# Kernel tuning notes

Measured on AMD Instinct MI355X. Metric: run time of the kernel, lower is better.

The kernel has to match this reference:

```python
import jax, jax.numpy as jnp
import numpy as np

B, CIN, COUT, H, W, K, PAD = 8, 64, 64, 128, 128, 3, 1
KK = K * K


def setup_inputs() -> dict:
    key = jax.random.key(0)
    k1, k2, k3, k4 = jax.random.split(key, 4)
    x = jax.random.normal(k1, (B, CIN, H, W), jnp.float32)
    # offset/mask conv: 3*K*K output channels (2*KK offsets + KK mask logits).
    # Original zero-inits these; we use small random weights so the irregular
    # gather path is actually exercised (zero offsets degenerate to plain conv).
    w_off = jax.random.normal(k2, (3 * KK, CIN, K, K), jnp.float32) * 0.01
    b_off = jax.random.normal(k3, (3 * KK,), jnp.float32) * 0.01
    w_dcn = jax.random.normal(k4, (COUT, CIN, K, K), jnp.float32) * (1.0 / np.sqrt(CIN * KK))
    return {"x": x, "w_off": w_off, "b_off": b_off, "w_dcn": w_dcn}


def _bilinear_gather(x, py, px):
    # x: [B,C,H,W]; py/px: [B,KK,H,W] float sample coordinates.
    # Zero padding: integer corners outside the image contribute 0 (torchvision semantics).
    Bn, C, Hn, Wn = x.shape
    y0 = jnp.floor(py).astype(jnp.int32)
    x0 = jnp.floor(px).astype(jnp.int32)
    y1, x1 = y0 + 1, x0 + 1
    wy1 = py - y0.astype(py.dtype)
    wy0 = 1.0 - wy1
    wx1 = px - x0.astype(px.dtype)
    wx0 = 1.0 - wx1
    xf = x.reshape(Bn, C, Hn * Wn)

    def g(iy, ix):
        valid = ((iy >= 0) & (iy < Hn) & (ix >= 0) & (ix < Wn)).astype(x.dtype)
        idx = (jnp.clip(iy, 0, Hn - 1) * Wn + jnp.clip(ix, 0, Wn - 1)).reshape(Bn, -1)
        v = jax.vmap(lambda xr, i: xr[:, i])(xf, idx).reshape(Bn, C, *iy.shape[1:])
        return v * valid[:, None]  # [B,C,KK,H,W]

    return ((wy0 * wx0)[:, None] * g(y0, x0) + (wy0 * wx1)[:, None] * g(y0, x1)
            + (wy1 * wx0)[:, None] * g(y1, x0) + (wy1 * wx1)[:, None] * g(y1, x1))


def reference(x, w_off, b_off, w_dcn):
    dn = ('NCHW', 'OIHW', 'NCHW')
    off = jax.lax.conv_general_dilated(x, w_off, (1, 1), [(PAD, PAD), (PAD, PAD)],
                                       dimension_numbers=dn) + b_off[None, :, None, None]
    o1, o2, m = off[:, :KK], off[:, KK:2 * KK], off[:, 2 * KK:]
    mask = jax.nn.sigmoid(m)                    # [B,KK,H,W]
    offset = jnp.concatenate([o1, o2], axis=1)  # [B,2KK,H,W], torch cat((o1,o2),dim=1)
    # torchvision interprets channel 2k as dy, 2k+1 as dx for kernel point k
    dy, dx = offset[:, 0::2], offset[:, 1::2]   # each [B,KK,H,W]
    ki = (jnp.arange(KK) // K - PAD).astype(x.dtype)
    kj = (jnp.arange(KK) % K - PAD).astype(x.dtype)
    py = jnp.arange(H, dtype=x.dtype)[None, None, :, None] + ki[None, :, None, None] + dy
    px = jnp.arange(W, dtype=x.dtype)[None, None, None, :] + kj[None, :, None, None] + dx
    val = _bilinear_gather(x, py, px) * mask[:, None]  # [B,C,KK,H,W]
    return jnp.einsum('bckhw,ock->bohw', val, w_dcn.reshape(COUT, CIN, KK))
```

## Files before the change

### kernel.cpp

```cpp
#include <hip/hip_runtime.h>

#define Bn 8
#define CINn 64
#define COUTn 64
#define Hn 128
#define Wn 128
#define KKn 9

typedef __attribute__((ext_vector_type(8))) short short8v;
typedef __attribute__((ext_vector_type(4))) float f32x4;

__device__ __forceinline__ unsigned short f2bf(float f) {
    unsigned u = __float_as_uint(f);
    unsigned r = (u + 0x7FFFu + ((u >> 16) & 1u)) >> 16;
    return (unsigned short)r;
}

__global__ void wdcn_prep(const float* __restrict__ w_dcn, unsigned short* __restrict__ w2) {
    int i = blockIdx.x * 256 + threadIdx.x;
    if (i >= COUTn * CINn * KKn) return;
    int c = i & 63;
    int o = (i >> 6) & 63;
    int k = i >> 12;
    w2[i] = f2bf(w_dcn[(o * CINn + c) * KKn + k]);
}

__global__ void woffprep(const float* __restrict__ w_off, unsigned short* __restrict__ wofft) {
    int i = blockIdx.x * 256 + threadIdx.x;
    if (i >= 9 * 32 * 64) return;
    int c   = i & 63;
    int ch  = (i >> 6) & 31;
    int tap = i >> 11;
    wofft[i] = (ch < 27) ? f2bf(w_off[(ch * 64 + c) * 9 + tap]) : (unsigned short)0;
}

__launch_bounds__(256)
__global__ void offconv_mfma(const float* __restrict__ x,
                             const unsigned short* __restrict__ wofft,
                             const float* __restrict__ b_off, float* __restrict__ off) {
    __shared__ alignas(16) unsigned short XT[2 * 130 * 64];

    int blk = blockIdx.x;
    blk = (blk & 7) * 64 + (blk >> 3);
    const int b  = blk >> 6, hp = blk & 63;
    const int r0 = hp * 2;
    const int t  = threadIdx.x;
    const int lane = t & 63, wv = t >> 6;
    const int r16 = lane & 15, sub = lane >> 4;
    const int sw = t & 127, chalf = t >> 7;

    f32x4 acc[2][4];
#pragma unroll
    for (int mt = 0; mt < 2; ++mt)
#pragma unroll
        for (int nt = 0; nt < 4; ++nt) acc[mt][nt] = (f32x4){0.f, 0.f, 0.f, 0.f};

    if (t < 128) {
        int rs = t >> 6, which = (t >> 5) & 1, cpair = t & 31;
        int wslot = which ? 129 : 0;
        int c0 = cpair * 2;
        *(unsigned*)&XT[((rs * 130 + wslot) << 6) + (((c0 >> 3) ^ (wslot & 7)) << 3) + (c0 & 7)] = 0;
    }

    const float* xbase = x + (((long)b * CINn) << 14);

    for (int di = 0; di < 3; ++di) {
        if (di) __syncthreads();
#pragma unroll
        for (int rs = 0; rs < 2; ++rs) {
            int y = r0 + rs + di - 1;
            bool inb = (y >= 0 && y < Hn);
            int yc = inb ? y : 0;
            const float* xr = xbase + (yc << 7) + sw;
            int wslot = sw + 1;
#pragma unroll 4
            for (int cp = 0; cp < 16; ++cp) {
                int c0 = (chalf * 16 + cp) * 2;
                unsigned v = 0;
                if (inb) {
                    float lo = xr[(long)c0 << 14];
                    float hi = xr[(long)(c0 + 1) << 14];
                    v = (unsigned)f2bf(lo) | ((unsigned)f2bf(hi) << 16);
                }
                *(unsigned*)&XT[((rs * 130 + wslot) << 6) + (((c0 >> 3) ^ (wslot & 7)) << 3) + (c0 & 7)] = v;
            }
        }
        __syncthreads();

#pragma unroll
        for (int dj = 0; dj < 3; ++dj) {
            int tap = di * 3 + dj;
#pragma unroll
            for (int kk = 0; kk < 2; ++kk) {
                short8v a0 = *(const short8v*)(wofft + ((tap * 32 +      r16) << 6) + ((kk * 4 + sub) << 3));
                short8v a1 = *(const short8v*)(wofft + ((tap * 32 + 16 + r16) << 6) + ((kk * 4 + sub) << 3));
                short8v bfr[4];
#pragma unroll
                for (int nt = 0; nt < 4; ++nt) {
                    int ntile = wv * 4 + nt;
                    int hsel = ntile >> 3, wbase = (ntile & 7) * 16;
                    int wslot = wbase + r16 + dj;
                    int cchunk = kk * 4 + sub;
                    bfr[nt] = *(const short8v*)&XT[((hsel * 130 + wslot) << 6) + ((cchunk ^ (wslot & 7)) << 3)];
                }
#pragma unroll
                for (int nt = 0; nt < 4; ++nt) {
                    acc[0][nt] = __builtin_amdgcn_mfma_f32_16x16x32_bf16(a0, bfr[nt], acc[0][nt], 0, 0, 0);
                    acc[1][nt] = __builtin_amdgcn_mfma_f32_16x16x32_bf16(a1, bfr[nt], acc[1][nt], 0, 0, 0);
                }
            }
        }
    }

#pragma unroll
    for (int mt = 0; mt < 2; ++mt)
#pragma unroll
        for (int nt = 0; nt < 4; ++nt) {
            int ntile = wv * 4 + nt;
            int hsel = ntile >> 3, w = (ntile & 7) * 16 + r16;
            int h = r0 + hsel;
#pragma unroll
            for (int r = 0; r < 4; ++r) {
                int ch = mt * 16 + sub * 4 + r;
                if (ch < 27)
                    off[(((long)(b * 27 + ch)) << 14) + (h << 7) + w] = acc[mt][nt][r] + b_off[ch];
            }
        }
}

__launch_bounds__(256)
__global__ void dcn_main(const float* __restrict__ x, const float* __restrict__ off,
                         const unsigned short* __restrict__ w2, float* __restrict__ out) {
    __shared__ alignas(16) unsigned short wlds[4096];
    __shared__ alignas(16) unsigned short vlds[8192];

    int blk = blockIdx.x;
    blk = (blk & 7) * 128 + (blk >> 3);
    const int b = blk >> 7, h = blk & 127;
    const int t = threadIdx.x;

    f32x4 acc[2][4];
#pragma unroll
    for (int ot = 0; ot < 2; ++ot)
#pragma unroll
        for (int pt = 0; pt < 4; ++pt)
            acc[ot][pt] = (f32x4){0.f, 0.f, 0.f, 0.f};

    const int lane  = t & 63;
    const int wv    = t >> 6;
    const int ohalf = wv & 1;
    const int phalf = wv >> 1;
    const int sub   = lane >> 4;
    const int r16   = lane & 15;
    const int gpos  = t & 127;
    const int cp0   = t >> 7;
    const float* xb = x + (((long)b * CINn) << 14);
    const float* offb = off + (((long)b * 27) << 14) + (h << 7) + gpos;

    for (int k = 0; k < KKn; ++k) {
        __syncthreads();

#pragma unroll
        for (int i = 0; i < 2; ++i) {
            int q  = t + 256 * i;
            int o  = q >> 3, ch = q & 7;
            short8v w8 = *(const short8v*)(w2 + (k << 12) + (q << 3));
            *(short8v*)&wlds[(o << 6) + ((ch ^ (o & 7)) << 3)] = w8;
        }

        float dy = offb[(long)(2 * k) << 14];
        float dx = offb[(long)(2 * k + 1) << 14];
        float m  = offb[(long)(18 + k) << 14];
        m = 1.f / (1.f + __expf(-m));
        float py = (float)(h + (k / 3) - 1) + dy;
        float px = (float)(gpos + (k % 3) - 1) + dx;
        float fy = floorf(py), fx = floorf(px);
        int y0 = (int)fy, x0 = (int)fx;
        int y1 = y0 + 1, x1 = x0 + 1;
        float wy1 = py - fy, wx1 = px - fx;
        float a0 = (y0 >= 0 && y0 < Hn) ? (1.f - wy1) * m : 0.f;
        float a1 = (y1 >= 0 && y1 < Hn) ? wy1 * m : 0.f;
        float b0 = (x0 >= 0 && x0 < Wn) ? (1.f - wx1) : 0.f;
        float b1 = (x1 >= 0 && x1 < Wn) ? wx1 : 0.f;
        int y0c = min(max(y0, 0), Hn - 1), y1c = min(max(y1, 0), Hn - 1);
        int x0c = min(max(x0, 0), Wn - 1), x1c = min(max(x1, 0), Wn - 1);
        int i00 = (y0c << 7) + x0c, i01 = (y0c << 7) + x1c;
        int i10 = (y1c << 7) + x0c, i11 = (y1c << 7) + x1c;

#pragma unroll 4
        for (int it = 0; it < 16; ++it) {
            int cpair = cp0 + 2 * it;
            const float* xc0 = xb + ((long)(2 * cpair) << 14);
            const float* xc1 = xc0 + 16384;
            float v000 = xc0[i00], v001 = xc0[i01], v010 = xc0[i10], v011 = xc0[i11];
            float v100 = xc1[i00], v101 = xc1[i01], v110 = xc1[i10], v111 = xc1[i11];
            float val0 = a0 * (b0 * v000 + b1 * v001) + a1 * (b0 * v010 + b1 * v011);
            float val1 = a0 * (b0 * v100 + b1 * v101) + a1 * (b0 * v110 + b1 * v111);
            unsigned pkd = (unsigned)f2bf(val0) | ((unsigned)f2bf(val1) << 16);
            int cs = (cpair >> 2) ^ (gpos & 7);
            *(unsigned*)&vlds[(gpos << 6) + (cs << 3) + ((cpair & 3) << 1)] = pkd;
        }
        __syncthreads();

#pragma unroll
        for (int kk = 0; kk < 2; ++kk) {
            const int cc = kk * 4 + sub;
            short8v af[2], bf[4];
#pragma unroll
            for (int ot = 0; ot < 2; ++ot) {
                int o = ohalf * 32 + ot * 16 + r16;
                af[ot] = *(const short8v*)&wlds[(o << 6) + ((cc ^ (o & 7)) << 3)];
            }
#pragma unroll
            for (int pt = 0; pt < 4; ++pt) {
                int pos = phalf * 64 + pt * 16 + r16;
                bf[pt] = *(const short8v*)&vlds[(pos << 6) + ((cc ^ (pos & 7)) << 3)];
            }
#pragma unroll
            for (int ot = 0; ot < 2; ++ot)
#pragma unroll
                for (int pt = 0; pt < 4; ++pt)
                    acc[ot][pt] = __builtin_amdgcn_mfma_f32_16x16x32_bf16(af[ot], bf[pt], acc[ot][pt], 0, 0, 0);
        }
    }

    const long obase = (((long)b * COUTn) << 14) + (h << 7);
#pragma unroll
    for (int ot = 0; ot < 2; ++ot)
#pragma unroll
        for (int pt = 0; pt < 4; ++pt) {
#pragma unroll
            for (int r = 0; r < 4; ++r) {
                int o   = ohalf * 32 + ot * 16 + sub * 4 + r;
                int pos = phalf * 64 + pt * 16 + r16;
                out[obase + ((long)o << 14) + pos] = acc[ot][pt][r];
            }
        }
}

extern "C" void kernel_launch(void* const* d_in, const int* in_sizes, int n_in,
                              void* d_out, int out_size, void* d_ws, size_t ws_size,
                              hipStream_t stream) {
    const float* x     = (const float*)d_in[0];
    const float* w_off = (const float*)d_in[1];
    const float* b_off = (const float*)d_in[2];
    const float* w_dcn = (const float*)d_in[3];
    float* out = (float*)d_out;

    unsigned short* w2    = (unsigned short*)d_ws;
    unsigned short* wofft = (unsigned short*)((char*)d_ws + 73728);
    float*          off   = (float*)((char*)d_ws + 110592);

    wdcn_prep<<<144, 256, 0, stream>>>(w_dcn, w2);
    woffprep<<<72, 256, 0, stream>>>(w_off, wofft);
    offconv_mfma<<<512, 256, 0, stream>>>(x, wofft, b_off, off);
    dcn_main<<<Bn * Hn, 256, 0, stream>>>(x, off, w2, out);
}
```

Before: 297.9 us.

## Pre-transpose input to channel-last bf16 and gather MFMA operands directly from global

Adds an xt_prep kernel that converts x into a bf16 NHWC-style layout, so each pixel's 64 channels sit contiguously. The offset conv and the main DCN kernel then load MFMA B fragments straight from global memory as 16-byte vectors. This removes the LDS staging, the barriers and the strided per-channel fp32 gathers. The offsets are also stored as bf16, and the bilinear interpolation runs per fragment lane. The cost is an extra transpose pass over x plus reduced precision for the offsets and the sampled inputs.

```diff
diff --git a/kernel.cpp b/kernel.cpp
--- a/kernel.cpp
+++ b/kernel.cpp
@@ -14,6 +14,35 @@
     unsigned u = __float_as_uint(f);
     unsigned r = (u + 0x7FFFu + ((u >> 16) & 1u)) >> 16;
     return (unsigned short)r;
+}
+__device__ __forceinline__ float bf2f(unsigned short u) {
+    return __uint_as_float(((unsigned)u) << 16);
+}
+
+__launch_bounds__(256)
+__global__ void xt_prep(const float* __restrict__ x, unsigned short* __restrict__ xt) {
+    __shared__ unsigned short tile[128 * 68];
+    const int blk = blockIdx.x;
+    const int b = blk >> 7, y = blk & 127;
+    const int t = threadIdx.x;
+    const float* xb = x + (((long)b * CINn) << 14) + (y << 7);
+#pragma unroll
+    for (int i = 0; i < 32; ++i) {
+        int e = i * 256 + t;
+        int c = e >> 7, xx = e & 127;
+        tile[xx * 68 + c] = f2bf(xb[((long)c << 14) + xx]);
+    }
+    __syncthreads();
+    unsigned short* dst = xt + ((long)(b * 128 + y) << 13);
+#pragma unroll
+    for (int i = 0; i < 4; ++i) {
+        int q = i * 256 + t;
+        int xx = q >> 3, j = q & 7;
+        const unsigned long long* src = (const unsigned long long*)&tile[xx * 68 + j * 8];
+        unsigned long long v0 = src[0], v1 = src[1];
+        unsigned long long* d = (unsigned long long*)&dst[q * 8];
+        d[0] = v0; d[1] = v1;
+    }
 }
 
 __global__ void wdcn_prep(const float* __restrict__ w_dcn, unsigned short* __restrict__ w2) {
@@ -35,11 +64,10 @@
 }
 
 __launch_bounds__(256)
-__global__ void offconv_mfma(const float* __restrict__ x,
-                             const unsigned short* __restrict__ wofft,
-                             const float* __restrict__ b_off, float* __restrict__ off) {
-    __shared__ alignas(16) unsigned short XT[2 * 130 * 64];
-
+__global__ void offconv_direct(const unsigned short* __restrict__ xt,
+                               const unsigned short* __restrict__ wofft,
+                               const float* __restrict__ b_off,
+                               unsigned short* __restrict__ offo) {
     int blk = blockIdx.x;
     blk = (blk & 7) * 64 + (blk >> 3);
     const int b  = blk >> 6, hp = blk & 63;
@@ -47,7 +75,7 @@
     const int t  = threadIdx.x;
     const int lane = t & 63, wv = t >> 6;
     const int r16 = lane & 15, sub = lane >> 4;
-    const int sw = t & 127, chalf = t >> 7;
+    const unsigned short* xtb = xt + ((long)b << 20);
 
     f32x4 acc[2][4];
 #pragma unroll
@@ -55,53 +83,28 @@
 #pragma unroll
         for (int nt = 0; nt < 4; ++nt) acc[mt][nt] = (f32x4){0.f, 0.f, 0.f, 0.f};
 
-    if (t < 128) {
-        int rs = t >> 6, which = (t >> 5) & 1, cpair = t & 31;
-        int wslot = which ? 129 : 0;
-        int c0 = cpair * 2;
-        *(unsigned*)&XT[((rs * 130 + wslot) << 6) + (((c0 >> 3) ^ (wslot & 7)) << 3) + (c0 & 7)] = 0;
-    }
-
-    const float* xbase = x + (((long)b * CINn) << 14);
-
+    const short8v zf = {0, 0, 0, 0, 0, 0, 0, 0};
+
+#pragma unroll
     for (int di = 0; di < 3; ++di) {
-        if (di) __syncthreads();
-#pragma unroll
-        for (int rs = 0; rs < 2; ++rs) {
-            int y = r0 + rs + di - 1;
-            bool inb = (y >= 0 && y < Hn);
-            int yc = inb ? y : 0;
-            const float* xr = xbase + (yc << 7) + sw;
-            int wslot = sw + 1;
-#pragma unroll 4
-            for (int cp = 0; cp < 16; ++cp) {
-                int c0 = (chalf * 16 + cp) * 2;
-                unsigned v = 0;
-                if (inb) {
-                    float lo = xr[(long)c0 << 14];
-                    float hi = xr[(long)(c0 + 1) << 14];
-                    v = (unsigned)f2bf(lo) | ((unsigned)f2bf(hi) << 16);
-                }
-                *(unsigned*)&XT[((rs * 130 + wslot) << 6) + (((c0 >> 3) ^ (wslot & 7)) << 3) + (c0 & 7)] = v;
-            }
-        }
-        __syncthreads();
-
 #pragma unroll
         for (int dj = 0; dj < 3; ++dj) {
-            int tap = di * 3 + dj;
+            const int tap = di * 3 + dj;
 #pragma unroll
             for (int kk = 0; kk < 2; ++kk) {
-                short8v a0 = *(const short8v*)(wofft + ((tap * 32 +      r16) << 6) + ((kk * 4 + sub) << 3));
-                short8v a1 = *(const short8v*)(wofft + ((tap * 32 + 16 + r16) << 6) + ((kk * 4 + sub) << 3));
+                const int cc8 = (kk * 4 + sub) << 3;
+                short8v a0 = *(const short8v*)(wofft + ((tap * 32 +      r16) << 6) + cc8);
+                short8v a1 = *(const short8v*)(wofft + ((tap * 32 + 16 + r16) << 6) + cc8);
                 short8v bfr[4];
 #pragma unroll
                 for (int nt = 0; nt < 4; ++nt) {
                     int ntile = wv * 4 + nt;
-                    int hsel = ntile >> 3, wbase = (ntile & 7) * 16;
-                    int wslot = wbase + r16 + dj;
-                    int cchunk = kk * 4 + sub;
-                    bfr[nt] = *(const short8v*)&XT[((hsel * 130 + wslot) << 6) + ((cchunk ^ (wslot & 7)) << 3)];
+                    int y = r0 + (ntile >> 3) + di - 1;
+                    int w = (ntile & 7) * 16 + r16 + dj - 1;
+                    bool valid = (y >= 0 && y < Hn && w >= 0 && w < Wn);
+                    int yc = valid ? y : 0, wc = valid ? w : 0;
+                    short8v v = *(const short8v*)(xtb + (yc << 13) + (wc << 6) + cc8);
+                    bfr[nt] = valid ? v : zf;
                 }
 #pragma unroll
                 for (int nt = 0; nt < 4; ++nt) {
@@ -117,27 +120,30 @@
 #pragma unroll
         for (int nt = 0; nt < 4; ++nt) {
             int ntile = wv * 4 + nt;
-            int hsel = ntile >> 3, w = (ntile & 7) * 16 + r16;
-            int h = r0 + hsel;
+            int h = r0 + (ntile >> 3), w = (ntile & 7) * 16 + r16;
 #pragma unroll
             for (int r = 0; r < 4; ++r) {
                 int ch = mt * 16 + sub * 4 + r;
                 if (ch < 27)
-                    off[(((long)(b * 27 + ch)) << 14) + (h << 7) + w] = acc[mt][nt][r] + b_off[ch];
+                    offo[(((long)(b * 27 + ch)) << 14) + (h << 7) + w] = f2bf(acc[mt][nt][r] + b_off[ch]);
             }
         }
 }
 
 __launch_bounds__(256)
-__global__ void dcn_main(const float* __restrict__ x, const float* __restrict__ off,
-                         const unsigned short* __restrict__ w2, float* __restrict__ out) {
-    __shared__ alignas(16) unsigned short wlds[4096];
-    __shared__ alignas(16) unsigned short vlds[8192];
-
+__global__ void dcn_direct(const unsigned short* __restrict__ xt,
+                           const unsigned short* __restrict__ offo,
+                           const unsigned short* __restrict__ w2,
+                           float* __restrict__ out) {
     int blk = blockIdx.x;
     blk = (blk & 7) * 128 + (blk >> 3);
     const int b = blk >> 7, h = blk & 127;
     const int t = threadIdx.x;
+    const int lane = t & 63, wv = t >> 6;
+    const int ohalf = wv & 1, phalf = wv >> 1;
+    const int r16 = lane & 15, sub = lane >> 4;
+    const unsigned short* xtb = xt + ((long)b << 20);
+    const unsigned short* ob  = offo + (((long)b * 27) << 14) + (h << 7);
 
     f32x4 acc[2][4];
 #pragma unroll
@@ -146,81 +152,69 @@
         for (int pt = 0; pt < 4; ++pt)
             acc[ot][pt] = (f32x4){0.f, 0.f, 0.f, 0.f};
 
-    const int lane  = t & 63;
-    const int wv    = t >> 6;
-    const int ohalf = wv & 1;
-    const int phalf = wv >> 1;
-    const int sub   = lane >> 4;
-    const int r16   = lane & 15;
-    const int gpos  = t & 127;
-    const int cp0   = t >> 7;
-    const float* xb = x + (((long)b * CINn) << 14);
-    const float* offb = off + (((long)b * 27) << 14) + (h << 7) + gpos;
-
     for (int k = 0; k < KKn; ++k) {
-        __syncthreads();
-
-#pragma unroll
-        for (int i = 0; i < 2; ++i) {
-            int q  = t + 256 * i;
-            int o  = q >> 3, ch = q & 7;
-            short8v w8 = *(const short8v*)(w2 + (k << 12) + (q << 3));
-            *(short8v*)&wlds[(o << 6) + ((ch ^ (o & 7)) << 3)] = w8;
-        }
-
-        float dy = offb[(long)(2 * k) << 14];
-        float dx = offb[(long)(2 * k + 1) << 14];
-        float m  = offb[(long)(18 + k) << 14];
-        m = 1.f / (1.f + __expf(-m));
-        float py = (float)(h + (k / 3) - 1) + dy;
-        float px = (float)(gpos + (k % 3) - 1) + dx;
-        float fy = floorf(py), fx = floorf(px);
-        int y0 = (int)fy, x0 = (int)fx;
-        int y1 = y0 + 1, x1 = x0 + 1;
-        float wy1 = py - fy, wx1 = px - fx;
-        float a0 = (y0 >= 0 && y0 < Hn) ? (1.f - wy1) * m : 0.f;
-        float a1 = (y1 >= 0 && y1 < Hn) ? wy1 * m : 0.f;
-        float b0 = (x0 >= 0 && x0 < Wn) ? (1.f - wx1) : 0.f;
-        float b1 = (x1 >= 0 && x1 < Wn) ? wx1 : 0.f;
-        int y0c = min(max(y0, 0), Hn - 1), y1c = min(max(y1, 0), Hn - 1);
-        int x0c = min(max(x0, 0), Wn - 1), x1c = min(max(x1, 0), Wn - 1);
-        int i00 = (y0c << 7) + x0c, i01 = (y0c << 7) + x1c;
-        int i10 = (y1c << 7) + x0c, i11 = (y1c << 7) + x1c;
-
-#pragma unroll 4
-        for (int it = 0; it < 16; ++it) {
-            int cpair = cp0 + 2 * it;
-            const float* xc0 = xb + ((long)(2 * cpair) << 14);
-            const float* xc1 = xc0 + 16384;
-            float v000 = xc0[i00], v001 = xc0[i01], v010 = xc0[i10], v011 = xc0[i11];
-            float v100 = xc1[i00], v101 = xc1[i01], v110 = xc1[i10], v111 = xc1[i11];
-            float val0 = a0 * (b0 * v000 + b1 * v001) + a1 * (b0 * v010 + b1 * v011);
-            float val1 = a0 * (b0 * v100 + b1 * v101) + a1 * (b0 * v110 + b1 * v111);
-            unsigned pkd = (unsigned)f2bf(val0) | ((unsigned)f2bf(val1) << 16);
-            int cs = (cpair >> 2) ^ (gpos & 7);
-            *(unsigned*)&vlds[(gpos << 6) + (cs << 3) + ((cpair & 3) << 1)] = pkd;
-        }
-        __syncthreads();
+        const int ky = k / 3 - 1, kx = k % 3 - 1;
+        int o00[4], o01[4], o10[4], o11[4];
+        float q00[4], q01[4], q10[4], q11[4];
+#pragma unroll
+        for (int pt = 0; pt < 4; ++pt) {
+            int pos = phalf * 64 + pt * 16 + r16;
+            float dy = bf2f(ob[((long)(2 * k) << 14) + pos]);
+            float dx = bf2f(ob[((long)(2 * k + 1) << 14) + pos]);
+            float m  = bf2f(ob[((long)(18 + k) << 14) + pos]);
+            m = 1.f / (1.f + __expf(-m));
+            float py = (float)(h + ky) + dy;
+            float px = (float)(pos + kx) + dx;
+            float fy = floorf(py), fx = floorf(px);
+            int y0 = (int)fy, x0 = (int)fx;
+            float wy1 = py - fy, wx1 = px - fx;
+            float a0 = (y0 >= 0     && y0 < Hn)     ? (1.f - wy1) * m : 0.f;
+            float a1 = (y0 + 1 >= 0 && y0 + 1 < Hn) ? wy1 * m         : 0.f;
+            float b0 = (x0 >= 0     && x0 < Wn)     ? (1.f - wx1)     : 0.f;
+            float b1 = (x0 + 1 >= 0 && x0 + 1 < Wn) ? wx1             : 0.f;
+            q00[pt] = a0 * b0; q01[pt] = a0 * b1; q10[pt] = a1 * b0; q11[pt] = a1 * b1;
+            int y0c = min(max(y0, 0), Hn - 1), y1c = min(max(y0 + 1, 0), Hn - 1);
+            int x0c = min(max(x0, 0), Wn - 1), x1c = min(max(x0 + 1, 0), Wn - 1);
+            o00[pt] = (y0c << 13) + (x0c << 6); o01[pt] = (y0c << 13) + (x1c << 6);
+            o10[pt] = (y1c << 13) + (x0c << 6); o11[pt] = (y1c << 13) + (x1c << 6);
+        }
 
 #pragma unroll
         for (int kk = 0; kk < 2; ++kk) {
-            const int cc = kk * 4 + sub;
-            short8v af[2], bf[4];
-#pragma unroll
-            for (int ot = 0; ot < 2; ++ot) {
-                int o = ohalf * 32 + ot * 16 + r16;
-                af[ot] = *(const short8v*)&wlds[(o << 6) + ((cc ^ (o & 7)) << 3)];
-            }
+            const int cc8 = (kk * 4 + sub) << 3;
+            short8v af[2];
+            af[0] = *(const short8v*)(w2 + (k << 12) + ((ohalf * 32 +      r16) << 6) + cc8);
+            af[1] = *(const short8v*)(w2 + (k << 12) + ((ohalf * 32 + 16 + r16) << 6) + cc8);
+            short8v bfr[4];
 #pragma unroll
             for (int pt = 0; pt < 4; ++pt) {
-                int pos = phalf * 64 + pt * 16 + r16;
-                bf[pt] = *(const short8v*)&vlds[(pos << 6) + ((cc ^ (pos & 7)) << 3)];
+                short8v c00 = *(const short8v*)(xtb + o00[pt] + cc8);
+                short8v c01 = *(const short8v*)(xtb + o01[pt] + cc8);
+                short8v c10 = *(const short8v*)(xtb + o10[pt] + cc8);
+                short8v c11 = *(const short8v*)(xtb + o11[pt] + cc8);
+                const unsigned* u00 = (const unsigned*)&c00;
+                const unsigned* u01 = (const unsigned*)&c01;
+                const unsigned* u10 = (const unsigned*)&c10;
+                const unsigned* u11 = (const unsigned*)&c11;
+                short8v bf;
+                unsigned* ub = (unsigned*)&bf;
+#pragma unroll
+                for (int jj = 0; jj < 4; ++jj) {
+                    float f00l = __uint_as_float(u00[jj] << 16), f00h = __uint_as_float(u00[jj] & 0xffff0000u);
+                    float f01l = __uint_as_float(u01[jj] << 16), f01h = __uint_as_float(u01[jj] & 0xffff0000u);
+                    float f10l = __uint_as_float(u10[jj] << 16), f10h = __uint_as_float(u10[jj] & 0xffff0000u);
+                    float f11l = __uint_as_float(u11[jj] << 16), f11h = __uint_as_float(u11[jj] & 0xffff0000u);
+                    float tl = q00[pt] * f00l + q01[pt] * f01l + q10[pt] * f10l + q11[pt] * f11l;
+                    float th = q00[pt] * f00h + q01[pt] * f01h + q10[pt] * f10h + q11[pt] * f11h;
+                    ub[jj] = (unsigned)f2bf(tl) | ((unsigned)f2bf(th) << 16);
+                }
+                bfr[pt] = bf;
             }
 #pragma unroll
             for (int ot = 0; ot < 2; ++ot)
 #pragma unroll
                 for (int pt = 0; pt < 4; ++pt)
-                    acc[ot][pt] = __builtin_amdgcn_mfma_f32_16x16x32_bf16(af[ot], bf[pt], acc[ot][pt], 0, 0, 0);
+                    acc[ot][pt] = __builtin_amdgcn_mfma_f32_16x16x32_bf16(af[ot], bfr[pt], acc[ot][pt], 0, 0, 0);
         }
     }
 
@@ -247,12 +241,14 @@
     const float* w_dcn = (const float*)d_in[3];
     float* out = (float*)d_out;
 
-    unsigned short* w2    = (unsigned short*)d_ws;
-    unsigned short* wofft = (unsigned short*)((char*)d_ws + 73728);
-    float*          off   = (float*)((char*)d_ws + 110592);
-
+    unsigned short* xt    = (unsigned short*)d_ws;
+    unsigned short* w2    = (unsigned short*)((char*)d_ws + 16777216);
+    unsigned short* wofft = (unsigned short*)((char*)d_ws + 16850944);
+    unsigned short* offo  = (unsigned short*)((char*)d_ws + 16887808);
+
+    xt_prep<<<Bn * Hn, 256, 0, stream>>>(x, xt);
     wdcn_prep<<<144, 256, 0, stream>>>(w_dcn, w2);
     woffprep<<<72, 256, 0, stream>>>(w_off, wofft);
-    offconv_mfma<<<512, 256, 0, stream>>>(x, wofft, b_off, off);
-    dcn_main<<<Bn * Hn, 256, 0, stream>>>(x, off, w2, out);
-}
+    offconv_direct<<<512, 256, 0, stream>>>(xt, wofft, b_off, offo);
+    dcn_direct<<<Bn * Hn, 256, 0, stream>>>(xt, offo, w2, out);
+}
```

Result: faster. 257.3 us (-13.6%).
